# Kernel tuning notes

Measured on AMD Instinct MI355X. Metric: run time of the kernel, lower is better.

Reference implementation:

```python
import jax, jax.numpy as jnp
import numpy as np

B = 524288          # replay batch size
NUM_ATOMS = 51      # C51 atoms
V_MIN = -10.0
V_MAX = 10.0
DISCOUNT = 0.99     # scalar `discount` arg of project(), closed over as a constant


def setup_inputs() -> dict:
    key = jax.random.key(0)
    k1, k2, k3 = jax.random.split(key, 3)
    # next_dist is a categorical distribution over atoms (softmax-normalized)
    logits = jax.random.normal(k1, (B, NUM_ATOMS), dtype=jnp.float32)
    next_dist = jax.nn.softmax(logits, axis=-1)
    rewards = jax.random.normal(k2, (B,), dtype=jnp.float32)
    bootstrap = (jax.random.uniform(k3, (B,)) > 0.1).astype(jnp.float32)
    return {"next_dist": next_dist, "rewards": rewards, "bootstrap": bootstrap}


def reference(next_dist, rewards, bootstrap):
    delta_z = (V_MAX - V_MIN) / (NUM_ATOMS - 1)
    q_support = jnp.linspace(V_MIN, V_MAX, NUM_ATOMS, dtype=jnp.float32)

    # Bellman-backed atom locations, clamped to support: [B, A]
    target_z = rewards[:, None] + bootstrap[:, None] * DISCOUNT * q_support
    target_z = jnp.clip(target_z, V_MIN, V_MAX)
    b = (target_z - V_MIN) / delta_z

    lower = jnp.floor(b).astype(jnp.int32)
    upper = jnp.ceil(b).astype(jnp.int32)

    # handle exact-integer bins (lower == upper) exactly as the torch code
    is_int = lower == upper
    l_mask = is_int & (lower > 0)
    u_mask = is_int & (lower == 0)
    lower = jnp.where(l_mask, lower - 1, lower)
    upper = jnp.where(u_mask, upper + 1, upper)

    # flattened dual scatter-add, row-local via per-row offset
    bsz = next_dist.shape[0]
    offset = (jnp.arange(bsz, dtype=jnp.int32) * NUM_ATOMS)[:, None]  # [B,1]
    l_idx = (lower + offset).reshape(-1)
    u_idx = (upper + offset).reshape(-1)
    w_l = (next_dist * (upper.astype(jnp.float32) - b)).reshape(-1)
    w_u = (next_dist * (b - lower.astype(jnp.float32))).reshape(-1)

    proj = jnp.zeros(bsz * NUM_ATOMS, dtype=next_dist.dtype)
    proj = proj.at[l_idx].add(w_l).at[u_idx].add(w_u)
    return proj.reshape(bsz, NUM_ATOMS)
```

## Files before the change

kernel.cpp:

```cpp
#include <hip/hip_runtime.h>


namespace {

constexpr int NA    = 51;
constexpr int BLOCK = 64;
constexpr int ELEMS = BLOCK * NA;
constexpr int VECS  = ELEMS / 4;

__global__ __launch_bounds__(BLOCK)
void c51_project(const float* __restrict__ next_dist,
                 const float* __restrict__ rewards,
                 const float* __restrict__ bootstrap,
                 float* __restrict__ out,
                 int B)
{
    __shared__ __align__(16) float lds[ELEMS];

    const int tid        = threadIdx.x;
    const int base_row   = blockIdx.x * BLOCK;
    const int rows_here  = min(BLOCK, B - base_row);
    const int elems_here = rows_here * NA;
    const long long base_elem = (long long)base_row * NA;

    float r = 0.0f, g = 0.0f;
    if (tid < rows_here) {
        r = rewards[base_row + tid];
        g = bootstrap[base_row + tid] * 0.99f;
    }

    if (elems_here == ELEMS) {
        const float4* __restrict__ in4 = (const float4*)(next_dist + base_elem);
        float4* l4 = (float4*)lds;
        #pragma unroll
        for (int v = tid; v < VECS; v += BLOCK) l4[v] = in4[v];
    } else {
        for (int e = tid; e < elems_here; e += BLOCK)
            lds[e] = next_dist[base_elem + e];
    }
    __syncthreads();

    if (tid < rows_here) {
        const int rb = tid * NA;

        float d[NA];
        #pragma unroll
        for (int j = 0; j < NA; ++j) d[j] = lds[rb + j];

        int   cur  = 0;
        float accL = 0.0f, accU = 0.0f;

        #pragma unroll
        for (int j = 0; j < NA; ++j) {
            const float z = fmaf((float)j, 0.4f, -10.0f);
            float t = fmaf(g, z, r);
            t = fminf(fmaxf(t, -10.0f), 10.0f);
            const float b = (t + 10.0f) * 2.5f;

            const float lf = floorf(b);
            int lower = (int)lf;
            if (b == lf && lower > 0) lower -= 1;

            const float wl = d[j] * ((float)(lower + 1) - b);
            const float wu = d[j] * (b - (float)lower);

            while (cur < lower) {
                lds[rb + cur] = accL;
                accL = accU;
                accU = 0.0f;
                ++cur;
            }
            accL += wl;
            accU += wu;
        }
        lds[rb + cur]     = accL;
        lds[rb + cur + 1] = accU;
        for (int k = cur + 2; k < NA; ++k) lds[rb + k] = 0.0f;
    }
    __syncthreads();

    if (elems_here == ELEMS) {
        float4* __restrict__ o4 = (float4*)(out + base_elem);
        const float4* __restrict__ a4 = (const float4*)lds;
        #pragma unroll
        for (int v = tid; v < VECS; v += BLOCK) o4[v] = a4[v];
    } else {
        for (int e = tid; e < elems_here; e += BLOCK)
            out[base_elem + e] = lds[e];
    }
}

}

extern "C" void kernel_launch(void* const* d_in, const int* in_sizes, int n_in,
                              void* d_out, int out_size, void* d_ws, size_t ws_size,
                              hipStream_t stream)
{
    const float* next_dist = (const float*)d_in[0];
    const float* rewards   = (const float*)d_in[1];
    const float* bootstrap = (const float*)d_in[2];
    float* out = (float*)d_out;

    const int B = in_sizes[1];
    const int nblocks = (B + BLOCK - 1) / BLOCK;

    c51_project<<<dim3(nblocks), dim3(BLOCK), 0, stream>>>(
        next_dist, rewards, bootstrap, out, B);
}
```

Before: 53.98 us.

## Process four row slabs per block with register-staged prefetch of next slab

Each workgroup now handles four consecutive 64-row slabs instead of one. The next slab's distribution is prefetched into registers while the current slab is scanned in LDS, so global load latency overlaps with compute. The grid shrinks fourfold and launch bounds now request a minimum occupancy of 3. The cost is fewer resident waves and higher register pressure from the 13-float4 staging buffer, which may hurt latency hiding in this memory-bound kernel.

Result: slower. 111.9 us (+107.3%).

```diff
diff --git a/kernel.cpp b/kernel.cpp
--- a/kernel.cpp
+++ b/kernel.cpp
@@ -5,10 +5,48 @@
 
 constexpr int NA    = 51;
 constexpr int BLOCK = 64;
-constexpr int ELEMS = BLOCK * NA;
+constexpr int ROWS  = 64;
+constexpr int NSLAB = 4;
+constexpr int ELEMS = ROWS * NA;
 constexpr int VECS  = ELEMS / 4;
+constexpr int VPL   = 13;
 
-__global__ __launch_bounds__(BLOCK)
+__device__ __forceinline__ void scan_row(float r, float g, int rb, float* lds)
+{
+    float d[NA];
+    #pragma unroll
+    for (int j = 0; j < NA; ++j) d[j] = lds[rb + j];
+
+    int   cur  = 0;
+    float accL = 0.0f, accU = 0.0f;
+
+    #pragma unroll
+    for (int j = 0; j < NA; ++j) {
+        const float z = fmaf((float)j, 0.4f, -10.0f);
+        float t = fmaf(g, z, r);
+        t = fminf(fmaxf(t, -10.0f), 10.0f);
+        const float b = (t + 10.0f) * 2.5f;
+
+        const float lf = floorf(b);
+        int lower = (int)lf;
+        if (b == lf && lower > 0) lower -= 1;
+
+        const float wl = d[j] * ((float)(lower + 1) - b);
+        const float wu = d[j] * (b - (float)lower);
+
+        while (cur < lower) {
+            lds[rb + cur] = accL;
+            accL = accU; accU = 0.0f; ++cur;
+        }
+        accL += wl;
+        accU += wu;
+    }
+    lds[rb + cur]     = accL;
+    lds[rb + cur + 1] = accU;
+    for (int k = cur + 2; k < NA; ++k) lds[rb + k] = 0.0f;
+}
+
+__global__ __launch_bounds__(BLOCK, 3)
 void c51_project(const float* __restrict__ next_dist,
                  const float* __restrict__ rewards,
                  const float* __restrict__ bootstrap,
@@ -17,76 +55,88 @@
 {
     __shared__ __align__(16) float lds[ELEMS];
 
-    const int tid        = threadIdx.x;
-    const int base_row   = blockIdx.x * BLOCK;
-    const int rows_here  = min(BLOCK, B - base_row);
-    const int elems_here = rows_here * NA;
-    const long long base_elem = (long long)base_row * NA;
+    const int tid = threadIdx.x;
+    const long long wg_row0 = (long long)blockIdx.x * (ROWS * NSLAB);
+    const bool wg_full = (wg_row0 + ROWS * NSLAB) <= (long long)B;
 
-    float r = 0.0f, g = 0.0f;
-    if (tid < rows_here) {
-        r = rewards[base_row + tid];
-        g = bootstrap[base_row + tid] * 0.99f;
-    }
+    if (wg_full) {
+        float r[NSLAB], g[NSLAB];
+        #pragma unroll
+        for (int k = 0; k < NSLAB; ++k) {
+            const long long row = wg_row0 + (long long)k * ROWS + tid;
+            r[k] = rewards[row];
+            g[k] = bootstrap[row] * 0.99f;
+        }
 
-    if (elems_here == ELEMS) {
-        const float4* __restrict__ in4 = (const float4*)(next_dist + base_elem);
-        float4* l4 = (float4*)lds;
-        #pragma unroll
-        for (int v = tid; v < VECS; v += BLOCK) l4[v] = in4[v];
-    } else {
-        for (int e = tid; e < elems_here; e += BLOCK)
-            lds[e] = next_dist[base_elem + e];
-    }
-    __syncthreads();
-
-    if (tid < rows_here) {
-        const int rb = tid * NA;
-
-        float d[NA];
-        #pragma unroll
-        for (int j = 0; j < NA; ++j) d[j] = lds[rb + j];
-
-        int   cur  = 0;
-        float accL = 0.0f, accU = 0.0f;
+        float4 stage[VPL];
+        {
+            const float4* __restrict__ in4 =
+                (const float4*)(next_dist + wg_row0 * NA);
+            #pragma unroll
+            for (int i = 0; i < VPL; ++i) {
+                const int v = tid + i * BLOCK;
+                if (v < VECS) stage[i] = in4[v];
+            }
+        }
 
         #pragma unroll
-        for (int j = 0; j < NA; ++j) {
-            const float z = fmaf((float)j, 0.4f, -10.0f);
-            float t = fmaf(g, z, r);
-            t = fminf(fmaxf(t, -10.0f), 10.0f);
-            const float b = (t + 10.0f) * 2.5f;
+        for (int k = 0; k < NSLAB; ++k) {
+            {
+                float4* l4 = (float4*)lds;
+                #pragma unroll
+                for (int i = 0; i < VPL; ++i) {
+                    const int v = tid + i * BLOCK;
+                    if (v < VECS) l4[v] = stage[i];
+                }
+            }
+            if (k + 1 < NSLAB) {
+                const float4* __restrict__ in4 =
+                    (const float4*)(next_dist + (wg_row0 + (long long)(k + 1) * ROWS) * NA);
+                #pragma unroll
+                for (int i = 0; i < VPL; ++i) {
+                    const int v = tid + i * BLOCK;
+                    if (v < VECS) stage[i] = in4[v];
+                }
+            }
+            __syncthreads();
 
-            const float lf = floorf(b);
-            int lower = (int)lf;
-            if (b == lf && lower > 0) lower -= 1;
+            scan_row(r[k], g[k], tid * NA, lds);
 
-            const float wl = d[j] * ((float)(lower + 1) - b);
-            const float wu = d[j] * (b - (float)lower);
+            __syncthreads();
 
-            while (cur < lower) {
-                lds[rb + cur] = accL;
-                accL = accU;
-                accU = 0.0f;
-                ++cur;
+            {
+                float4* __restrict__ o4 =
+                    (float4*)(out + (wg_row0 + (long long)k * ROWS) * NA);
+                const float4* __restrict__ a4 = (const float4*)lds;
+                #pragma unroll
+                for (int i = 0; i < VPL; ++i) {
+                    const int v = tid + i * BLOCK;
+                    if (v < VECS) o4[v] = a4[v];
+                }
             }
-            accL += wl;
-            accU += wu;
         }
-        lds[rb + cur]     = accL;
-        lds[rb + cur + 1] = accU;
-        for (int k = cur + 2; k < NA; ++k) lds[rb + k] = 0.0f;
-    }
-    __syncthreads();
+    } else {
+        for (int k = 0; k < NSLAB; ++k) {
+            const long long base_row = wg_row0 + (long long)k * ROWS;
+            const int rows_here = (int)min((long long)ROWS, (long long)B - base_row);
+            if (rows_here <= 0) break;
+            const int elems_here = rows_here * NA;
+            const long long base_elem = base_row * NA;
 
-    if (elems_here == ELEMS) {
-        float4* __restrict__ o4 = (float4*)(out + base_elem);
-        const float4* __restrict__ a4 = (const float4*)lds;
-        #pragma unroll
-        for (int v = tid; v < VECS; v += BLOCK) o4[v] = a4[v];
-    } else {
-        for (int e = tid; e < elems_here; e += BLOCK)
-            out[base_elem + e] = lds[e];
+            float r = 0.0f, g = 0.0f;
+            if (tid < rows_here) {
+                r = rewards[base_row + tid];
+                g = bootstrap[base_row + tid] * 0.99f;
+            }
+            for (int e = tid; e < elems_here; e += BLOCK)
+                lds[e] = next_dist[base_elem + e];
+            __syncthreads();
+            if (tid < rows_here) scan_row(r, g, tid * NA, lds);
+            __syncthreads();
+            for (int e = tid; e < elems_here; e += BLOCK)
+                out[base_elem + e] = lds[e];
+            __syncthreads();
+        }
     }
 }
 
@@ -102,7 +152,8 @@
     float* out = (float*)d_out;
 
     const int B = in_sizes[1];
-    const int nblocks = (B + BLOCK - 1) / BLOCK;
+    const int rows_per_wg = ROWS * NSLAB;
+    const int nblocks = (B + rows_per_wg - 1) / rows_per_wg;
 
     c51_project<<<dim3(nblocks), dim3(BLOCK), 0, stream>>>(
         next_dist, rewards, bootstrap, out, B);
```
